# Kernel optimization log

Measured on AMD Instinct MI355X. Metric: run time of the kernel, lower is better.

## Reference

```python
import jax, jax.numpy as jnp
import numpy as np

B, S, I, H = 128, 512, 256, 512


def _lstm_last_hidden(x, W_ih, W_hh, b_ih, b_hh):
    """Single-layer unidirectional LSTM (PyTorch gate order i,f,g,o).
    x: [B,S,I]; returns final hidden state h_n [B,H]."""
    Hd = W_hh.shape[1]
    # Precompute input-side gate activations for all timesteps: [S,B,4H]
    xg = jnp.einsum('bsi,gi->sbg', x, W_ih) + b_ih + b_hh

    def step(carry, gx):
        h, c = carry
        g = gx + h @ W_hh.T  # [B,4H]
        i, f, gg, o = jnp.split(g, 4, axis=-1)
        i = jax.nn.sigmoid(i)
        f = jax.nn.sigmoid(f)
        gg = jnp.tanh(gg)
        o = jax.nn.sigmoid(o)
        c = f * c + i * gg
        h = o * jnp.tanh(c)
        return (h, c), None

    h0 = jnp.zeros((x.shape[0], Hd), x.dtype)
    (h_n, _), _ = jax.lax.scan(step, (h0, h0), xg)
    return h_n


def setup_inputs() -> dict:
    key = jax.random.key(0)
    k1, k2, k3, k4, k5, k6 = jax.random.split(key, 6)
    s = 1.0 / np.sqrt(H)  # PyTorch LSTM init scale
    return {
        'text_one': jax.random.normal(k1, (B, S, I), jnp.float32),
        'text_two': jax.random.normal(k2, (B, S, I), jnp.float32),
        'W_ih': jax.random.normal(k3, (4 * H, I), jnp.float32) * s,
        'W_hh': jax.random.normal(k4, (4 * H, H), jnp.float32) * s,
        'b_ih': jax.random.normal(k5, (4 * H,), jnp.float32) * s,
        'b_hh': jax.random.normal(k6, (4 * H,), jnp.float32) * s,
    }


def reference(text_one, text_two, W_ih, W_hh, b_ih, b_hh):
    out1 = _lstm_last_hidden(text_one, W_ih, W_hh, b_ih, b_hh)
    out2 = _lstm_last_hidden(text_two, W_ih, W_hh, b_ih, b_hh)
    return (out1, out2)
```

## Files before the change

kernel.cpp:

```cpp
#include <hip/hip_runtime.h>
#include <stdint.h>

#define SLEN    512
#define IDIM    256
#define HDIM    512
#define NROW    256
#define HPH     520
#define XPF     260
#define NSTEP   512
#define NGRP    16
#define GWG     16

typedef __attribute__((ext_vector_type(8))) _Float16 half8;
typedef __attribute__((ext_vector_type(4))) float   f32x4;

#define AS1 __attribute__((address_space(1)))
#define AS3 __attribute__((address_space(3)))

__device__ __forceinline__ float sigm(float x)   { return 1.0f / (1.0f + __expf(-x)); }
__device__ __forceinline__ float tanh_f(float x) { return 2.0f / (1.0f + __expf(-2.0f * x)) - 1.0f; }

__device__ __forceinline__ half8 cvt8(float4 a, float4 b) {
    half8 v;
    v[0] = (_Float16)a.x; v[1] = (_Float16)a.y; v[2] = (_Float16)a.z; v[3] = (_Float16)a.w;
    v[4] = (_Float16)b.x; v[5] = (_Float16)b.y; v[6] = (_Float16)b.z; v[7] = (_Float16)b.w;
    return v;
}

union hu { _Float16 h; unsigned short u; };

__global__ __launch_bounds__(256, 1)
void lstm_persistent(const float* __restrict__ x0, const float* __restrict__ x1,
                     const float* __restrict__ wih, const float* __restrict__ whh,
                     const float* __restrict__ bih, const float* __restrict__ bhh,
                     _Float16* __restrict__ hb, int* __restrict__ flg,
                     float* __restrict__ out) {
    __shared__ __align__(16) _Float16 Hb[2][16 * HPH];
    __shared__ __align__(16) float    Xb[2][16 * XPF];

    const int tid  = threadIdx.x;
    const int lane = tid & 63;
    const int w    = tid >> 6;
    const int quad = lane >> 4;
    const int l16  = lane & 15;
    const int igrp = blockIdx.x & 15;
    const int jcg  = blockIdx.x >> 4;

    const int q0  = l16 & 3, ccl = l16 >> 2;
    const int colb = jcg * 32 + w * 8 + ccl * 2;
    const int gc0 = q0 * HDIM + colb;
    const int gc1 = gc0 + 1;
    half8 wf0[24], wf1[24];
#pragma unroll
    for (int kk = 0; kk < 24; ++kk) {
        int k0 = kk * 32 + quad * 8;
        const float* sA = (k0 < IDIM) ? wih + (size_t)gc0 * IDIM + k0
                                      : whh + (size_t)gc0 * HDIM + (k0 - IDIM);
        const float* sB = (k0 < IDIM) ? wih + (size_t)gc1 * IDIM + k0
                                      : whh + (size_t)gc1 * HDIM + (k0 - IDIM);
        wf0[kk] = cvt8(*(const float4*)sA, *(const float4*)(sA + 4));
        wf1[kk] = cvt8(*(const float4*)sB, *(const float4*)(sB + 4));
    }

    float bias0[4], bias1[4];
#pragma unroll
    for (int q = 0; q < 4; ++q) {
        int g0 = q * HDIM + jcg * 32 + w * 8 + quad * 2;
        bias0[q] = bih[g0] + bhh[g0];
        bias1[q] = bih[g0 + 1] + bhh[g0 + 1];
    }

    const float* xp  = (igrp < 8) ? x0 : x1;
    const int   brow = (igrp & 7) * 16;
    const int   grow = igrp * 16 + l16;
    const int   cc0  = jcg * 32 + w * 8 + quad * 2;

    const int* fpoll = flg + igrp * 64 + lane;
    int*       fmine = flg + igrp * 64 + jcg * 4 + w;

    float c0 = 0.f, c1 = 0.f;
    int gaveup = 0;

    half8 xf[8];
    {
#pragma unroll
        for (int p = 0; p < 4; ++p) {
            const int r = p * 4 + w;
            const float* g = xp + (size_t)(brow + r) * SLEN * IDIM + lane * 4;
            __builtin_amdgcn_global_load_lds(
                (const AS1 void*)g, (AS3 void*)&Xb[0][r * XPF], 16, 0, 0);
        }
        asm volatile("s_waitcnt vmcnt(0)" ::: "memory");
        __builtin_amdgcn_sched_barrier(0);
        __builtin_amdgcn_s_barrier();
        const float* xb = &Xb[0][l16 * XPF + quad * 8];
#pragma unroll
        for (int kk = 0; kk < 8; ++kk)
            xf[kk] = cvt8(*(const float4*)(xb + kk * 32),
                          *(const float4*)(xb + kk * 32 + 4));
    }

#pragma unroll 1
    for (int t = 0; t < NSTEP; ++t) {
        int f0 = 0;
        if (t > 0) {
            asm volatile("global_load_dword %0, %1, off sc0 sc1"
                         : "=&v"(f0) : "v"(fpoll) : "memory");
            __builtin_amdgcn_sched_barrier(0);
        }

        f32x4 acc0 = {bias0[0], bias0[1], bias0[2], bias0[3]};
        f32x4 acc1 = {bias1[0], bias1[1], bias1[2], bias1[3]};
#pragma unroll
        for (int kk = 0; kk < 8; ++kk) {
            acc0 = __builtin_amdgcn_mfma_f32_16x16x32_f16(wf0[kk], xf[kk], acc0, 0, 0, 0);
            acc1 = __builtin_amdgcn_mfma_f32_16x16x32_f16(wf1[kk], xf[kk], acc1, 0, 0, 0);
        }
        __builtin_amdgcn_sched_barrier(0);

        if (t > 0 && !gaveup) {
            asm volatile("s_waitcnt vmcnt(0)" ::: "memory");
            __builtin_amdgcn_sched_barrier(0);
            if (!__all(f0 >= t)) {
                int it = 0;
                while (true) {
                    int f;
                    asm volatile("global_load_dword %0, %1, off sc0 sc1\n\t"
                                 "s_waitcnt vmcnt(0)"
                                 : "=&v"(f) : "v"(fpoll) : "memory");
                    if (__all(f >= t)) break;
                    __builtin_amdgcn_s_sleep(1);
                    if (++it > (1 << 20)) { gaveup = 1; break; }
                }
            }
            __builtin_amdgcn_fence(__ATOMIC_ACQUIRE, "workgroup");
        }

        {
            const _Float16* hsrc = hb + (size_t)((t + 1) & 1) * (NROW * HDIM)
                                      + (size_t)(igrp * 16) * HDIM;
#pragma unroll
            for (int p = 0; p < 4; ++p) {
                const int r = p * 4 + w;
                __builtin_amdgcn_global_load_lds(
                    (const AS1 void*)(hsrc + (size_t)r * HDIM + lane * 8),
                    (AS3 void*)&Hb[t & 1][r * HPH], 16, 0, 17);
            }
            if (t < NSTEP - 1) {
#pragma unroll
                for (int p = 0; p < 4; ++p) {
                    const int r = p * 4 + w;
                    const float* g = xp + (size_t)(brow + r) * SLEN * IDIM
                                        + (size_t)(t + 1) * IDIM + lane * 4;
                    __builtin_amdgcn_global_load_lds(
                        (const AS1 void*)g, (AS3 void*)&Xb[(t + 1) & 1][r * XPF],
                        16, 0, 0);
                }
            }
        }
        asm volatile("s_waitcnt vmcnt(0)" ::: "memory");
        __builtin_amdgcn_sched_barrier(0);
        __builtin_amdgcn_s_barrier();

        {
            const _Float16* abh = &Hb[t & 1][l16 * HPH + quad * 8];
            f32x4 b0 = {0.f, 0.f, 0.f, 0.f}, b1 = {0.f, 0.f, 0.f, 0.f};
#pragma unroll
            for (int kk = 0; kk < 16; kk += 2) {
                half8 bfa = *(const half8*)(abh + kk * 32);
                half8 bfb = *(const half8*)(abh + (kk + 1) * 32);
                acc0 = __builtin_amdgcn_mfma_f32_16x16x32_f16(wf0[8 + kk], bfa, acc0, 0, 0, 0);
                b0   = __builtin_amdgcn_mfma_f32_16x16x32_f16(wf0[9 + kk], bfb, b0, 0, 0, 0);
                acc1 = __builtin_amdgcn_mfma_f32_16x16x32_f16(wf1[8 + kk], bfa, acc1, 0, 0, 0);
                b1   = __builtin_amdgcn_mfma_f32_16x16x32_f16(wf1[9 + kk], bfb, b1, 0, 0, 0);
            }
            acc0 += b0;
            acc1 += b1;
        }

        float i0 = sigm(acc0[0]), f0g = sigm(acc0[1]), g0 = tanh_f(acc0[2]), o0g = sigm(acc0[3]);
        c0 = f0g * c0 + i0 * g0;
        float h0 = o0g * tanh_f(c0);
        float i1 = sigm(acc1[0]), f1g = sigm(acc1[1]), g1 = tanh_f(acc1[2]), o1g = sigm(acc1[3]);
        c1 = f1g * c1 + i1 * g1;
        float h1 = o1g * tanh_f(c1);

        if (t < NSTEP - 1) {
            _Float16* hd = hb + (size_t)(t & 1) * (NROW * HDIM) + (size_t)grow * HDIM;
            hu u0; u0.h = (_Float16)h0;
            hu u1; u1.h = (_Float16)h1;
            unsigned int hp = (unsigned int)u0.u | ((unsigned int)u1.u << 16);
            asm volatile("global_store_dword %0, %1, off sc0 sc1"
                         :: "v"((int*)(hd + cc0)), "v"(hp) : "memory");
            __builtin_amdgcn_sched_barrier(0);
            asm volatile("s_waitcnt vmcnt(0)" ::: "memory");
            __builtin_amdgcn_sched_barrier(0);
            if (lane == 0) {
                int fv = t + 1;
                asm volatile("global_store_dword %0, %1, off sc0 sc1"
                             :: "v"(fmine), "v"(fv) : "memory");
            }
            const float* xb = &Xb[(t + 1) & 1][l16 * XPF + quad * 8];
#pragma unroll
            for (int kk = 0; kk < 8; ++kk)
                xf[kk] = cvt8(*(const float4*)(xb + kk * 32),
                              *(const float4*)(xb + kk * 32 + 4));
        } else {
            float2 ov; ov.x = h0; ov.y = h1;
            *(float2*)(out + (size_t)grow * HDIM + cc0) = ov;
        }
    }
}

extern "C" void kernel_launch(void* const* d_in, const int* in_sizes, int n_in,
                              void* d_out, int out_size, void* d_ws, size_t ws_size,
                              hipStream_t stream) {
    const float* x0  = (const float*)d_in[0];
    const float* x1  = (const float*)d_in[1];
    const float* wih = (const float*)d_in[2];
    const float* whh = (const float*)d_in[3];
    const float* bih = (const float*)d_in[4];
    const float* bhh = (const float*)d_in[5];

    _Float16* hb = (_Float16*)d_ws;
    int* flg = (int*)((char*)d_ws + (size_t)2 * NROW * HDIM * sizeof(_Float16));
    size_t zbytes = (size_t)2 * NROW * HDIM * sizeof(_Float16)
                  + (size_t)NGRP * 64 * sizeof(int);
    hipMemsetAsync(d_ws, 0, zbytes, stream);

    lstm_persistent<<<dim3(256), dim3(256), 0, stream>>>(
        x0, x1, wih, whh, bih, bhh, hb, flg, (float*)d_out);
}
```

Measured before the change: 1.749 ms.

## Add dedicated producer wavefront for flag polling and H/X loads

Adds a fifth wavefront per block that polls the cross-block flags and issues all global-to-LDS loads of the previous hidden state and next input slice. The four compute waves now only synchronize on workgroup barriers. The input-projection MFMAs for the next step are moved to the end of the previous step, so they run off the critical path. This separates polling and memory latency from the compute waves. In exchange, the barrier handshake becomes more complex, and one wave serially issues four times as many loads.

```diff
diff --git a/kernel.cpp b/kernel.cpp
--- a/kernel.cpp
+++ b/kernel.cpp
@@ -29,7 +29,7 @@
 
 union hu { _Float16 h; unsigned short u; };
 
-__global__ __launch_bounds__(256, 1)
+__global__ __launch_bounds__(320, 1)
 void lstm_persistent(const float* __restrict__ x0, const float* __restrict__ x1,
                      const float* __restrict__ wih, const float* __restrict__ whh,
                      const float* __restrict__ bih, const float* __restrict__ bhh,
@@ -46,46 +46,15 @@
     const int igrp = blockIdx.x & 15;
     const int jcg  = blockIdx.x >> 4;
 
-    const int q0  = l16 & 3, ccl = l16 >> 2;
-    const int colb = jcg * 32 + w * 8 + ccl * 2;
-    const int gc0 = q0 * HDIM + colb;
-    const int gc1 = gc0 + 1;
-    half8 wf0[24], wf1[24];
-#pragma unroll
-    for (int kk = 0; kk < 24; ++kk) {
-        int k0 = kk * 32 + quad * 8;
-        const float* sA = (k0 < IDIM) ? wih + (size_t)gc0 * IDIM + k0
-                                      : whh + (size_t)gc0 * HDIM + (k0 - IDIM);
-        const float* sB = (k0 < IDIM) ? wih + (size_t)gc1 * IDIM + k0
-                                      : whh + (size_t)gc1 * HDIM + (k0 - IDIM);
-        wf0[kk] = cvt8(*(const float4*)sA, *(const float4*)(sA + 4));
-        wf1[kk] = cvt8(*(const float4*)sB, *(const float4*)(sB + 4));
-    }
-
-    float bias0[4], bias1[4];
-#pragma unroll
-    for (int q = 0; q < 4; ++q) {
-        int g0 = q * HDIM + jcg * 32 + w * 8 + quad * 2;
-        bias0[q] = bih[g0] + bhh[g0];
-        bias1[q] = bih[g0 + 1] + bhh[g0 + 1];
-    }
-
     const float* xp  = (igrp < 8) ? x0 : x1;
     const int   brow = (igrp & 7) * 16;
-    const int   grow = igrp * 16 + l16;
-    const int   cc0  = jcg * 32 + w * 8 + quad * 2;
-
-    const int* fpoll = flg + igrp * 64 + lane;
-    int*       fmine = flg + igrp * 64 + jcg * 4 + w;
-
-    float c0 = 0.f, c1 = 0.f;
-    int gaveup = 0;
-
-    half8 xf[8];
-    {
-#pragma unroll
-        for (int p = 0; p < 4; ++p) {
-            const int r = p * 4 + w;
+
+    if (w == 4) {
+        const int* fpoll = flg + igrp * 64 + lane;
+        int gaveup = 0;
+
+#pragma unroll
+        for (int r = 0; r < 16; ++r) {
             const float* g = xp + (size_t)(brow + r) * SLEN * IDIM + lane * 4;
             __builtin_amdgcn_global_load_lds(
                 (const AS1 void*)g, (AS3 void*)&Xb[0][r * XPF], 16, 0, 0);
@@ -93,35 +62,10 @@
         asm volatile("s_waitcnt vmcnt(0)" ::: "memory");
         __builtin_amdgcn_sched_barrier(0);
         __builtin_amdgcn_s_barrier();
-        const float* xb = &Xb[0][l16 * XPF + quad * 8];
-#pragma unroll
-        for (int kk = 0; kk < 8; ++kk)
-            xf[kk] = cvt8(*(const float4*)(xb + kk * 32),
-                          *(const float4*)(xb + kk * 32 + 4));
-    }
 
 #pragma unroll 1
-    for (int t = 0; t < NSTEP; ++t) {
-        int f0 = 0;
-        if (t > 0) {
-            asm volatile("global_load_dword %0, %1, off sc0 sc1"
-                         : "=&v"(f0) : "v"(fpoll) : "memory");
-            __builtin_amdgcn_sched_barrier(0);
-        }
-
-        f32x4 acc0 = {bias0[0], bias0[1], bias0[2], bias0[3]};
-        f32x4 acc1 = {bias1[0], bias1[1], bias1[2], bias1[3]};
-#pragma unroll
-        for (int kk = 0; kk < 8; ++kk) {
-            acc0 = __builtin_amdgcn_mfma_f32_16x16x32_f16(wf0[kk], xf[kk], acc0, 0, 0, 0);
-            acc1 = __builtin_amdgcn_mfma_f32_16x16x32_f16(wf1[kk], xf[kk], acc1, 0, 0, 0);
-        }
-        __builtin_amdgcn_sched_barrier(0);
-
-        if (t > 0 && !gaveup) {
-            asm volatile("s_waitcnt vmcnt(0)" ::: "memory");
-            __builtin_amdgcn_sched_barrier(0);
-            if (!__all(f0 >= t)) {
+        for (int t = 0; t < NSTEP; ++t) {
+            if (t > 0 && !gaveup) {
                 int it = 0;
                 while (true) {
                     int f;
@@ -132,24 +76,21 @@
                     __builtin_amdgcn_s_sleep(1);
                     if (++it > (1 << 20)) { gaveup = 1; break; }
                 }
-            }
-            __builtin_amdgcn_fence(__ATOMIC_ACQUIRE, "workgroup");
-        }
-
-        {
-            const _Float16* hsrc = hb + (size_t)((t + 1) & 1) * (NROW * HDIM)
-                                      + (size_t)(igrp * 16) * HDIM;
-#pragma unroll
-            for (int p = 0; p < 4; ++p) {
-                const int r = p * 4 + w;
-                __builtin_amdgcn_global_load_lds(
-                    (const AS1 void*)(hsrc + (size_t)r * HDIM + lane * 8),
-                    (AS3 void*)&Hb[t & 1][r * HPH], 16, 0, 17);
+                __builtin_amdgcn_fence(__ATOMIC_ACQUIRE, "workgroup");
+            }
+            {
+                const _Float16* hsrc = hb + (size_t)((t + 1) & 1) * (NROW * HDIM)
+                                          + (size_t)(igrp * 16) * HDIM;
+#pragma unroll
+                for (int r = 0; r < 16; ++r) {
+                    __builtin_amdgcn_global_load_lds(
+                        (const AS1 void*)(hsrc + (size_t)r * HDIM + lane * 8),
+                        (AS3 void*)&Hb[t & 1][r * HPH], 16, 0, 17);
+                }
             }
             if (t < NSTEP - 1) {
 #pragma unroll
-                for (int p = 0; p < 4; ++p) {
-                    const int r = p * 4 + w;
+                for (int r = 0; r < 16; ++r) {
                     const float* g = xp + (size_t)(brow + r) * SLEN * IDIM
                                         + (size_t)(t + 1) * IDIM + lane * 4;
                     __builtin_amdgcn_global_load_lds(
@@ -157,9 +98,64 @@
                         16, 0, 0);
                 }
             }
-        }
-        asm volatile("s_waitcnt vmcnt(0)" ::: "memory");
-        __builtin_amdgcn_sched_barrier(0);
+            asm volatile("s_waitcnt vmcnt(0)" ::: "memory");
+            __builtin_amdgcn_sched_barrier(0);
+            __builtin_amdgcn_s_barrier();
+        }
+        return;
+    }
+
+    const int q0  = l16 & 3, ccl = l16 >> 2;
+    const int colb = jcg * 32 + w * 8 + ccl * 2;
+    const int gc0 = q0 * HDIM + colb;
+    const int gc1 = gc0 + 1;
+    half8 wf0[24], wf1[24];
+#pragma unroll
+    for (int kk = 0; kk < 24; ++kk) {
+        int k0 = kk * 32 + quad * 8;
+        const float* sA = (k0 < IDIM) ? wih + (size_t)gc0 * IDIM + k0
+                                      : whh + (size_t)gc0 * HDIM + (k0 - IDIM);
+        const float* sB = (k0 < IDIM) ? wih + (size_t)gc1 * IDIM + k0
+                                      : whh + (size_t)gc1 * HDIM + (k0 - IDIM);
+        wf0[kk] = cvt8(*(const float4*)sA, *(const float4*)(sA + 4));
+        wf1[kk] = cvt8(*(const float4*)sB, *(const float4*)(sB + 4));
+    }
+
+    float bias0[4], bias1[4];
+#pragma unroll
+    for (int q = 0; q < 4; ++q) {
+        int g0 = q * HDIM + jcg * 32 + w * 8 + quad * 2;
+        bias0[q] = bih[g0] + bhh[g0];
+        bias1[q] = bih[g0 + 1] + bhh[g0 + 1];
+    }
+
+    const int grow = igrp * 16 + l16;
+    const int cc0  = jcg * 32 + w * 8 + quad * 2;
+    int*      fmine = flg + igrp * 64 + jcg * 4 + w;
+
+    float c0 = 0.f, c1 = 0.f;
+
+    __builtin_amdgcn_s_barrier();
+
+    half8 xf[8];
+    f32x4 acc0, acc1;
+    {
+        const float* xb = &Xb[0][l16 * XPF + quad * 8];
+#pragma unroll
+        for (int kk = 0; kk < 8; ++kk)
+            xf[kk] = cvt8(*(const float4*)(xb + kk * 32),
+                          *(const float4*)(xb + kk * 32 + 4));
+        acc0 = f32x4{bias0[0], bias0[1], bias0[2], bias0[3]};
+        acc1 = f32x4{bias1[0], bias1[1], bias1[2], bias1[3]};
+#pragma unroll
+        for (int kk = 0; kk < 8; ++kk) {
+            acc0 = __builtin_amdgcn_mfma_f32_16x16x32_f16(wf0[kk], xf[kk], acc0, 0, 0, 0);
+            acc1 = __builtin_amdgcn_mfma_f32_16x16x32_f16(wf1[kk], xf[kk], acc1, 0, 0, 0);
+        }
+    }
+
+#pragma unroll 1
+    for (int t = 0; t < NSTEP; ++t) {
         __builtin_amdgcn_s_barrier();
 
         {
@@ -205,6 +201,13 @@
             for (int kk = 0; kk < 8; ++kk)
                 xf[kk] = cvt8(*(const float4*)(xb + kk * 32),
                               *(const float4*)(xb + kk * 32 + 4));
+            acc0 = f32x4{bias0[0], bias0[1], bias0[2], bias0[3]};
+            acc1 = f32x4{bias1[0], bias1[1], bias1[2], bias1[3]};
+#pragma unroll
+            for (int kk = 0; kk < 8; ++kk) {
+                acc0 = __builtin_amdgcn_mfma_f32_16x16x32_f16(wf0[kk], xf[kk], acc0, 0, 0, 0);
+                acc1 = __builtin_amdgcn_mfma_f32_16x16x32_f16(wf1[kk], xf[kk], acc1, 0, 0, 0);
+            }
         } else {
             float2 ov; ov.x = h0; ov.y = h1;
             *(float2*)(out + (size_t)grow * HDIM + cc0) = ov;
@@ -228,6 +231,6 @@
                   + (size_t)NGRP * 64 * sizeof(int);
     hipMemsetAsync(d_ws, 0, zbytes, stream);
 
-    lstm_persistent<<<dim3(256), dim3(256), 0, stream>>>(
+    lstm_persistent<<<dim3(256), dim3(320), 0, stream>>>(
         x0, x1, wih, whh, bih, bhh, hb, flg, (float*)d_out);
 }
```

Result: slower. 2.702 ms (+54.5%).
